# Kernel optimization log

Measured on AMD Instinct MI355X. Metric: run time of the kernel, lower is better.

The kernel has to match this reference:

```python
import jax, jax.numpy as jnp
import numpy as np


def setup_inputs() -> dict:
    key = jax.random.key(0)
    k1, k2, k3, k4 = jax.random.split(key, 4)
    B, I, P, F = 4096, 1024, 512, 2048
    x = jax.random.normal(k1, (B, I), dtype=jnp.float32)
    # params initialized like torch.rand(...)*2-1 (uniform in [-1,1])
    features = jax.random.uniform(k2, (F, I), dtype=jnp.float32, minval=-1.0, maxval=1.0)
    prototypes = jax.random.uniform(k3, (P, I), dtype=jnp.float32, minval=-1.0, maxval=1.0)
    # scalars: torch inits to zeros; use small nonzero values so output/grads are informative
    abt = jax.random.normal(k4, (3,), dtype=jnp.float32) * 0.1
    alpha = abt[0:1]
    beta = abt[1:2]
    theta = abt[2:3]
    return {"x": x, "features": features, "prototypes": prototypes,
            "alpha": alpha, "beta": beta, "theta": theta}


def reference(x, features, prototypes, alpha, beta, theta):
    # x: [b, i], features: [f, i], prototypes: [p, i]
    # Original einsums broadcast over p but the projection is p-independent:
    xf = x @ features.T            # [b, f]
    pf = prototypes @ features.T   # [p, f]
    x_pres = jax.nn.relu(xf)       # [b, f]
    p_pres = jax.nn.relu(pf)       # [p, f]
    # common[b,p]       = sum_f xf*pf*relu(xf)*relu(pf)
    # x_distinct[b,p]   = sum_f xf*relu(xf)*(1-relu(pf))
    # p_distinct[b,p]   = sum_f pf*relu(pf)*(1-relu(xf))
    a = xf * x_pres                # [b, f]
    c = pf * p_pres                # [p, f]
    common = a @ c.T                                   # [b, p]
    x_distinctive = a @ (1.0 - p_pres).T               # [b, p]
    p_distinctive = (1.0 - x_pres) @ c.T               # [b, p]
    return theta * common - alpha * x_distinctive - beta * p_distinctive
```

## Files before the change

kernel.cpp:

```cpp
#include <hip/hip_runtime.h>
#include <cstdint>

typedef __attribute__((ext_vector_type(8))) short bf16x8;
typedef __attribute__((ext_vector_type(16))) float f32x16;
typedef __attribute__((ext_vector_type(4))) float f4;
typedef __attribute__((ext_vector_type(8))) unsigned short u16x8;
typedef unsigned short u16;


__device__ __forceinline__ u16 f2bf(float f) {
  uint32_t u = __builtin_bit_cast(uint32_t, f);
  u += 0x7fffu + ((u >> 16) & 1u);
  return (u16)(u >> 16);
}

__device__ __forceinline__ float bf2f(u16 h) {
  return __builtin_bit_cast(float, (uint32_t)h << 16);
}

__device__ __forceinline__ void async_cp16(const void* g, void* l) {
  __builtin_amdgcn_global_load_lds(
      (const __attribute__((address_space(1))) uint32_t*)g,
      (__attribute__((address_space(3))) uint32_t*)l, 16, 0, 0);
}

__global__ __launch_bounds__(256) void cast3(
    const float* __restrict__ x, const float* __restrict__ f,
    const float* __restrict__ p, u16* __restrict__ dst,
    int n1, int n2, int n3) {
  int i = (blockIdx.x * 256 + threadIdx.x) * 8;
  const float* src;
  int local;
  if (i < n1) { src = x; local = i; }
  else if (i < n1 + n2) { src = f; local = i - n1; }
  else if (i < n1 + n2 + n3) { src = p; local = i - n1 - n2; }
  else return;
  f4 a = *(const f4*)(src + local);
  f4 b = *(const f4*)(src + local + 4);
  u16x8 o;
  o[0] = f2bf(a.x); o[1] = f2bf(a.y); o[2] = f2bf(a.z); o[3] = f2bf(a.w);
  o[4] = f2bf(b.x); o[5] = f2bf(b.y); o[6] = f2bf(b.z); o[7] = f2bf(b.w);
  *(u16x8*)(dst + i) = o;
}


__device__ __forceinline__ void stage_tile(
    const u16* __restrict__ A, const u16* __restrict__ B, int K,
    int k0, int tid, u16* L) {
  constexpr int TM = 128, TN = 128;
  const int wave = tid >> 6;
  #pragma unroll
  for (int it = 0; it < TM / 32; ++it) {
    int c = it * 256 + tid;
    int row = c >> 3, pc = c & 7;
    int gc = pc ^ (row & 7);
    async_cp16(A + (size_t)row * K + (k0 + gc * 8),
               &L[(it * 256 + wave * 64) * 8]);
  }
  #pragma unroll
  for (int it = 0; it < TN / 32; ++it) {
    int c = it * 256 + tid;
    int row = c >> 3, pc = c & 7;
    int gc = pc ^ (row & 7);
    async_cp16(B + (size_t)row * K + (k0 + gc * 8),
               &L[TM * 64 + (it * 256 + wave * 64) * 8]);
  }
}

__device__ __forceinline__ void compute_tile(
    const u16* L, int lane, int wrow, int wcol, f32x16 (&acc)[2][2]) {
  constexpr int TM = 128;
  #pragma unroll
  for (int s = 0; s < 4; ++s) {
    const int h = s * 2 + (lane >> 5);
    bf16x8 bfr[2], afr[2];
    #pragma unroll
    for (int j = 0; j < 2; ++j) {
      const int rb = wcol * 64 + j * 32 + (lane & 31);
      bfr[j] = *(const bf16x8*)&L[TM * 64 + (rb * 8 + (h ^ (rb & 7))) * 8];
    }
    #pragma unroll
    for (int i = 0; i < 2; ++i) {
      const int ra = wrow * 64 + i * 32 + (lane & 31);
      afr[i] = *(const bf16x8*)&L[(ra * 8 + (h ^ (ra & 7))) * 8];
    }
    #pragma unroll
    for (int i = 0; i < 2; ++i)
      #pragma unroll
      for (int j = 0; j < 2; ++j)
        acc[i][j] = __builtin_amdgcn_mfma_f32_32x32x16_bf16(
            afr[i], bfr[j], acc[i][j], 0, 0, 0);
  }
}

__device__ __forceinline__ void mainloop(
    const u16* __restrict__ A, const u16* __restrict__ B, int K,
    int kbeg, int kend, int tid, u16* lds, f32x16 (&acc)[2][2]) {
  constexpr int BK = 64;
  constexpr int BUF = 16384;
  const int lane = tid & 63;
  const int wave = tid >> 6;
  const int wrow = wave >> 1, wcol = wave & 1;

  stage_tile(A, B, K, kbeg, tid, lds);
  int cur = 0;
  for (int k0 = kbeg; k0 < kend; k0 += BK) {
    if (k0 + BK < kend) {
      stage_tile(A, B, K, k0 + BK, tid, lds + (cur ^ 1) * BUF);
      asm volatile("s_waitcnt vmcnt(8)" ::: "memory");
    } else {
      asm volatile("s_waitcnt vmcnt(0)" ::: "memory");
    }
    __builtin_amdgcn_s_barrier();
    compute_tile(lds + cur * BUF, lane, wrow, wcol, acc);
    __builtin_amdgcn_s_barrier();
    cur ^= 1;
  }
}


__device__ __forceinline__ void stage_tile256(
    const u16* __restrict__ A, const u16* __restrict__ B, int K,
    int k0, int tid, u16* L) {
  const int wave = tid >> 6;
  #pragma unroll
  for (int it = 0; it < 4; ++it) {
    int c = it * 512 + tid;
    int row = c >> 3, pc = c & 7;
    int gc = pc ^ (row & 7);
    async_cp16(A + (size_t)row * K + (k0 + gc * 8),
               &L[(it * 512 + wave * 64) * 8]);
  }
  #pragma unroll
  for (int it = 0; it < 4; ++it) {
    int c = it * 512 + tid;
    int row = c >> 3, pc = c & 7;
    int gc = pc ^ (row & 7);
    async_cp16(B + (size_t)row * K + (k0 + gc * 8),
               &L[16384 + (it * 512 + wave * 64) * 8]);
  }
}

__device__ __forceinline__ void compute_tile256(
    const u16* L, int lane, int wrow, int wcol, f32x16 (&acc)[4][2]) {
  #pragma unroll
  for (int s = 0; s < 4; ++s) {
    const int h = s * 2 + (lane >> 5);
    bf16x8 bfr[2], afr[4];
    #pragma unroll
    for (int j = 0; j < 2; ++j) {
      const int rb = wcol * 64 + j * 32 + (lane & 31);
      bfr[j] = *(const bf16x8*)&L[16384 + (rb * 8 + (h ^ (rb & 7))) * 8];
    }
    #pragma unroll
    for (int i = 0; i < 4; ++i) {
      const int ra = wrow * 128 + i * 32 + (lane & 31);
      afr[i] = *(const bf16x8*)&L[(ra * 8 + (h ^ (ra & 7))) * 8];
    }
    #pragma unroll
    for (int i = 0; i < 4; ++i)
      #pragma unroll
      for (int j = 0; j < 2; ++j)
        acc[i][j] = __builtin_amdgcn_mfma_f32_32x32x16_bf16(
            afr[i], bfr[j], acc[i][j], 0, 0, 0);
  }
}

__device__ __forceinline__ void mainloop256(
    const u16* __restrict__ A, const u16* __restrict__ B, int K,
    int kbeg, int kend, int tid, u16* lds, f32x16 (&acc)[4][2]) {
  constexpr int BK = 64;
  constexpr int BUF = 32768;
  const int lane = tid & 63;
  const int wave = tid >> 6;
  const int wrow = wave >> 2, wcol = wave & 3;

  stage_tile256(A, B, K, kbeg, tid, lds);
  int cur = 0;
  for (int k0 = kbeg; k0 < kend; k0 += BK) {
    if (k0 + BK < kend) {
      stage_tile256(A, B, K, k0 + BK, tid, lds + (cur ^ 1) * BUF);
      asm volatile("s_waitcnt vmcnt(8)" ::: "memory");
    } else {
      asm volatile("s_waitcnt vmcnt(0)" ::: "memory");
    }
    __builtin_amdgcn_s_barrier();
    compute_tile256(lds + cur * BUF, lane, wrow, wcol, acc);
    __builtin_amdgcn_s_barrier();
    cur ^= 1;
  }
}


__global__ __launch_bounds__(256) void gemm12(
    const u16* __restrict__ xb, const u16* __restrict__ pb,
    const u16* __restrict__ fb, u16* __restrict__ Acat, u16* __restrict__ Bcat,
    const float* __restrict__ alpha, const float* __restrict__ beta,
    const float* __restrict__ theta) {
  constexpr int TM = 128, K = 1024, N = 2048;
  constexpr int TSTRIDE = 136;
  __shared__ u16 lds[32768];

  const int tid = threadIdx.x;
  const int lane = tid & 63;
  const int wave = tid >> 6;
  const int wrow = wave >> 1, wcol = wave & 1;

  const int bid = blockIdx.x;
  const int xcd = bid & 7, slot = bid >> 3;
  const int xt = (xcd & 3) * 9 + (slot >> 3);
  const int yt = (xcd >> 2) * 8 + (slot & 7);

  const int bm_all = xt * TM;
  const int bn = yt * 128;
  const bool is_x = bm_all < 4096;
  const u16* A = is_x ? xb + (size_t)bm_all * K : pb + (size_t)(bm_all - 4096) * K;
  const u16* B = fb + (size_t)bn * K;

  f32x16 acc[2][2] = {};
  mainloop(A, B, K, 0, K, tid, lds, acc);

  float th = 0.f, al = 0.f, be = 0.f;
  if (!is_x) { th = theta[0]; al = alpha[0]; be = beta[0]; }
  u16* dst = is_x ? Acat : Bcat;
  const int rowbase = is_x ? bm_all : bm_all - 4096;
  const int rquad = 4 * (lane >> 5);

  #pragma unroll
  for (int half = 0; half < 2; ++half) {
    __syncthreads();
    #pragma unroll
    for (int i = 0; i < 2; ++i) {
      #pragma unroll
      for (int j = 0; j < 2; ++j) {
        const int cl = wcol * 64 + j * 32 + (lane & 31);
        #pragma unroll
        for (int r = 0; r < 16; ++r) {
          const int rl = wrow * 64 + i * 32 + (r & 3) + 8 * (r >> 2) + rquad;
          float v = acc[i][j][r];
          float pres = v > 0.f ? v : 0.f;
          float o;
          if (is_x) o = half == 0 ? v * pres : 1.f - pres;
          else {
            float cc = v * pres;
            o = half == 0 ? th * cc - al * (1.f - pres) : -be * cc;
          }
          lds[rl * TSTRIDE + cl] = f2bf(o);
        }
      }
    }
    __syncthreads();
    #pragma unroll
    for (int v = 0; v < 8; ++v) {
      const int rl = v * 16 + (tid >> 4);
      const int c8 = (tid & 15) * 8;
      u16x8 vec = *(const u16x8*)&lds[rl * TSTRIDE + c8];
      *(u16x8*)&dst[(size_t)(rowbase + rl) * (2 * N) + bn + c8 + half * N] = vec;
    }
  }
}

__global__ __launch_bounds__(512) void gemm3(
    const u16* __restrict__ Acat, const u16* __restrict__ Bcat,
    u16* __restrict__ part) {
  constexpr int K = 4096, KSPLIT = 8;
  __shared__ u16 lds[65536];

  const int tid = threadIdx.x;
  const int bid = blockIdx.x;
  const int bz = bid & 7;
  const int slot = bid >> 3;
  const int bxt = slot & 15;
  const int byt = slot >> 4;

  const int bm = bxt * 256;
  const int bn = byt * 256;
  const int kbeg = bz * (K / KSPLIT);
  const int kend = kbeg + (K / KSPLIT);

  f32x16 acc[4][2] = {};
  mainloop256(Acat + (size_t)bm * K, Bcat + (size_t)bn * K, K, kbeg, kend,
              tid, lds, acc);

  const int tileId = byt * 16 + bxt;
  const size_t pbase = ((size_t)bz * 32 + tileId) * 65536;
  #pragma unroll
  for (int i = 0; i < 4; ++i)
    #pragma unroll
    for (int j = 0; j < 2; ++j)
      #pragma unroll
      for (int h = 0; h < 2; ++h) {
        u16x8 o;
        #pragma unroll
        for (int e = 0; e < 8; ++e) o[e] = f2bf(acc[i][j][h * 8 + e]);
        *(u16x8*)&part[pbase + (size_t)(i * 4 + j * 2 + h) * 4096 + tid * 8] = o;
      }
}

__global__ __launch_bounds__(512) void reduce4(
    const u16* __restrict__ part, float* __restrict__ out) {
  constexpr int N = 512;
  const int tid = threadIdx.x;
  const int lane = tid & 63;
  const int wave = tid >> 6;
  const int wrow = wave >> 2, wcol = wave & 3;
  const int tileId = blockIdx.x >> 4;
  const int q = blockIdx.x & 15;
  const int bm = (tileId & 15) * 256;
  const int bn = (tileId >> 4) * 256;

  float v[8] = {};
  #pragma unroll
  for (int z = 0; z < 8; ++z) {
    u16x8 u = *(const u16x8*)&part[((size_t)z * 32 + tileId) * 65536 +
                                   (size_t)q * 4096 + tid * 8];
    #pragma unroll
    for (int e = 0; e < 8; ++e) v[e] += bf2f(u[e]);
  }
  const int i = q >> 2, j = (q >> 1) & 1, h = q & 1;
  const int gc = bn + wcol * 64 + j * 32 + (lane & 31);
  const int grb = bm + wrow * 128 + i * 32 + 4 * (lane >> 5);
  #pragma unroll
  for (int e = 0; e < 8; ++e) {
    const int reg = h * 8 + e;
    out[(size_t)(grb + (reg & 3) + 8 * (reg >> 2)) * N + gc] = v[e];
  }
}

extern "C" void kernel_launch(void* const* d_in, const int* in_sizes, int n_in,
                              void* d_out, int out_size, void* d_ws, size_t ws_size,
                              hipStream_t stream) {
  const float* x     = (const float*)d_in[0];
  const float* feat  = (const float*)d_in[1];
  const float* proto = (const float*)d_in[2];
  const float* alpha = (const float*)d_in[3];
  const float* beta  = (const float*)d_in[4];
  const float* theta = (const float*)d_in[5];
  float* out = (float*)d_out;

  constexpr int Bb = 4096, Ii = 1024, Pp = 512, Ff = 2048;

  char* ws = (char*)d_ws;
  u16* xb   = (u16*)ws;
  u16* fb   = xb + (size_t)Bb * Ii;
  u16* pb   = fb + (size_t)Ff * Ii;
  size_t r0 = 33554432;
  u16* Acat = (u16*)(ws + r0);
  u16* Bcat = Acat + (size_t)Bb * 2 * Ff;
  u16* part = Bcat + (size_t)Pp * 2 * Ff;

  const int n1 = Bb * Ii, n2 = Ff * Ii, n3 = Pp * Ii;
  cast3<<<((n1 + n2 + n3) / 8 + 255) / 256, 256, 0, stream>>>(
      x, feat, proto, xb, n1, n2, n3);

  gemm12<<<576, 256, 0, stream>>>(xb, pb, fb, Acat, Bcat, alpha, beta, theta);

  gemm3<<<256, 512, 0, stream>>>(Acat, Bcat, part);

  reduce4<<<512, 512, 0, stream>>>(part, out);
}
```

Before: 138.2 us.

## Restructure gemm3 mainloop into 4-stage BK=32 pipeline with interleaved loads

```diff
diff --git a/kernel.cpp b/kernel.cpp
--- a/kernel.cpp
+++ b/kernel.cpp
@@ -119,75 +119,75 @@
 }
 
 
-__device__ __forceinline__ void stage_tile256(
+__device__ __forceinline__ void stage_unit32(
+    const u16* __restrict__ M, int K, int k0, int tid, u16* Lbase) {
+  #pragma unroll
+  for (int it = 0; it < 2; ++it) {
+    int c = it * 512 + tid;
+    int row = c >> 2, pc = c & 3;
+    int gc = pc ^ ((row >> 1) & 3);
+    async_cp16(M + (size_t)row * K + (k0 + gc * 8),
+               &Lbase[(it * 512 + (tid >> 6) * 64) * 8]);
+  }
+}
+
+__device__ __forceinline__ void mainloop32(
     const u16* __restrict__ A, const u16* __restrict__ B, int K,
-    int k0, int tid, u16* L) {
-  const int wave = tid >> 6;
-  #pragma unroll
-  for (int it = 0; it < 4; ++it) {
-    int c = it * 512 + tid;
-    int row = c >> 3, pc = c & 7;
-    int gc = pc ^ (row & 7);
-    async_cp16(A + (size_t)row * K + (k0 + gc * 8),
-               &L[(it * 512 + wave * 64) * 8]);
-  }
-  #pragma unroll
-  for (int it = 0; it < 4; ++it) {
-    int c = it * 512 + tid;
-    int row = c >> 3, pc = c & 7;
-    int gc = pc ^ (row & 7);
-    async_cp16(B + (size_t)row * K + (k0 + gc * 8),
-               &L[16384 + (it * 512 + wave * 64) * 8]);
-  }
-}
-
-__device__ __forceinline__ void compute_tile256(
-    const u16* L, int lane, int wrow, int wcol, f32x16 (&acc)[4][2]) {
-  #pragma unroll
-  for (int s = 0; s < 4; ++s) {
-    const int h = s * 2 + (lane >> 5);
-    bf16x8 bfr[2], afr[4];
-    #pragma unroll
-    for (int j = 0; j < 2; ++j) {
-      const int rb = wcol * 64 + j * 32 + (lane & 31);
-      bfr[j] = *(const bf16x8*)&L[16384 + (rb * 8 + (h ^ (rb & 7))) * 8];
-    }
-    #pragma unroll
-    for (int i = 0; i < 4; ++i) {
-      const int ra = wrow * 128 + i * 32 + (lane & 31);
-      afr[i] = *(const bf16x8*)&L[(ra * 8 + (h ^ (ra & 7))) * 8];
-    }
-    #pragma unroll
-    for (int i = 0; i < 4; ++i)
-      #pragma unroll
-      for (int j = 0; j < 2; ++j)
-        acc[i][j] = __builtin_amdgcn_mfma_f32_32x32x16_bf16(
-            afr[i], bfr[j], acc[i][j], 0, 0, 0);
-  }
-}
-
-__device__ __forceinline__ void mainloop256(
-    const u16* __restrict__ A, const u16* __restrict__ B, int K,
-    int kbeg, int kend, int tid, u16* lds, f32x16 (&acc)[4][2]) {
-  constexpr int BK = 64;
-  constexpr int BUF = 32768;
+    int kbeg, int tid, u16* lds, f32x16 (&acc)[4][2]) {
+  constexpr int NT = 16;
+  constexpr int BUFS = 16384;
   const int lane = tid & 63;
   const int wave = tid >> 6;
   const int wrow = wave >> 2, wcol = wave & 3;
 
-  stage_tile256(A, B, K, kbeg, tid, lds);
-  int cur = 0;
-  for (int k0 = kbeg; k0 < kend; k0 += BK) {
-    if (k0 + BK < kend) {
-      stage_tile256(A, B, K, k0 + BK, tid, lds + (cur ^ 1) * BUF);
-      asm volatile("s_waitcnt vmcnt(8)" ::: "memory");
-    } else {
-      asm volatile("s_waitcnt vmcnt(0)" ::: "memory");
-    }
-    __builtin_amdgcn_s_barrier();
-    compute_tile256(lds + cur * BUF, lane, wrow, wcol, acc);
-    __builtin_amdgcn_s_barrier();
-    cur ^= 1;
+  #pragma unroll
+  for (int p = 0; p < 3; ++p) {
+    stage_unit32(A, K, kbeg + p * 32, tid, lds + p * BUFS);
+    stage_unit32(B, K, kbeg + p * 32, tid, lds + p * BUFS + 8192);
+  }
+  asm volatile("s_waitcnt vmcnt(8)" ::: "memory");
+  __builtin_amdgcn_s_barrier();
+
+  for (int t = 0; t < NT; ++t) {
+    const u16* L = lds + (t & 3) * BUFS;
+    u16* Lnxt = lds + ((t + 3) & 3) * BUFS;
+    const int k3 = kbeg + (t + 3) * 32;
+    #pragma unroll
+    for (int s = 0; s < 2; ++s) {
+      const int h = s * 2 + (lane >> 5);
+      bf16x8 bfr[2], afr[4];
+      #pragma unroll
+      for (int j = 0; j < 2; ++j) {
+        const int rb = wcol * 64 + j * 32 + (lane & 31);
+        bfr[j] = *(const bf16x8*)&L[8192 + (rb * 4 + (h ^ ((rb >> 1) & 3))) * 8];
+      }
+      #pragma unroll
+      for (int i = 0; i < 4; ++i) {
+        const int ra = wrow * 128 + i * 32 + (lane & 31);
+        afr[i] = *(const bf16x8*)&L[(ra * 4 + (h ^ ((ra >> 1) & 3))) * 8];
+      }
+      if (t < NT - 3) {
+        if (s == 0) stage_unit32(A, K, k3, tid, Lnxt);
+        else        stage_unit32(B, K, k3, tid, Lnxt + 8192);
+      }
+      __builtin_amdgcn_s_barrier();
+      asm volatile("s_waitcnt lgkmcnt(0)" ::: "memory");
+      __builtin_amdgcn_sched_barrier(0);
+      __builtin_amdgcn_s_setprio(1);
+      #pragma unroll
+      for (int i = 0; i < 4; ++i)
+        #pragma unroll
+        for (int j = 0; j < 2; ++j)
+          acc[i][j] = __builtin_amdgcn_mfma_f32_32x32x16_bf16(
+              afr[i], bfr[j], acc[i][j], 0, 0, 0);
+      __builtin_amdgcn_s_setprio(0);
+      if (s == 1) {
+        if (t < NT - 3)       asm volatile("s_waitcnt vmcnt(8)" ::: "memory");
+        else if (t == NT - 3) asm volatile("s_waitcnt vmcnt(4)" ::: "memory");
+        else if (t == NT - 2) asm volatile("s_waitcnt vmcnt(0)" ::: "memory");
+      }
+      __builtin_amdgcn_s_barrier();
+    }
   }
 }
 
@@ -276,11 +276,10 @@
   const int bm = bxt * 256;
   const int bn = byt * 256;
   const int kbeg = bz * (K / KSPLIT);
-  const int kend = kbeg + (K / KSPLIT);
 
   f32x16 acc[4][2] = {};
-  mainloop256(Acat + (size_t)bm * K, Bcat + (size_t)bn * K, K, kbeg, kend,
-              tid, lds, acc);
+  mainloop32(Acat + (size_t)bm * K, Bcat + (size_t)bn * K, K, kbeg,
+             tid, lds, acc);
 
   const int tileId = byt * 16 + bxt;
   const size_t pbase = ((size_t)bz * 32 + tileId) * 65536;
```

After: 142.5 us. 3.1% more time.
